# Performance work log

Hardware: AMD Instinct MI355X
Metric: run time of the kernel (lower is better)

The kernel has to match this reference:

```python
import jax, jax.numpy as jnp
import numpy as np

C = 64
EPS = 1e-5


def conv3x3(x, w, groups=1):
    # x: NCHW, w: OIHW, stride 1, padding 1, dilation 1 (matches the torch code)
    return jax.lax.conv_general_dilated(
        x, w, window_strides=(1, 1), padding=((1, 1), (1, 1)),
        dimension_numbers=('NCHW', 'OIHW', 'NCHW'), feature_group_count=groups)


def shared_conv(x, w_shared):
    # SharedConv: one (1,1,3,3) filter applied to every channel == depthwise conv
    # with the weight broadcast across channels (replaces the per-channel loop).
    w = jnp.broadcast_to(w_shared, (C, 1, 3, 3))
    return conv3x3(x, w, groups=C)


def sdc(x, w_sh, w_d, b_d):
    s = shared_conv(x, w_sh)
    d = conv3x3(s + x, w_d) + b_d[None, :, None, None]
    return d + x


def batch_norm(x, gamma, beta):
    # training-mode BatchNorm2d: batch statistics over (N, H, W), biased var
    mean = jnp.mean(x, axis=(0, 2, 3), keepdims=True)
    var = jnp.var(x, axis=(0, 2, 3), keepdims=True)
    xn = (x - mean) * jax.lax.rsqrt(var + EPS)
    return gamma[None, :, None, None] * xn + beta[None, :, None, None]


def setup_inputs() -> dict:
    key = jax.random.key(0)
    ks = jax.random.split(key, 7)
    fan_sh = 1 * 3 * 3
    fan_d = C * 3 * 3
    inp = {
        'x': jax.random.normal(ks[0], (4, C, 224, 224), dtype=jnp.float32),
        'w_sh1': jax.random.normal(ks[1], (1, 1, 3, 3), dtype=jnp.float32) / np.sqrt(fan_sh),
        'w_d1': jax.random.normal(ks[2], (C, C, 3, 3), dtype=jnp.float32) / np.sqrt(fan_d),
        'b_d1': jnp.zeros((C,), dtype=jnp.float32),
        'w_sh2': jax.random.normal(ks[3], (1, 1, 3, 3), dtype=jnp.float32) / np.sqrt(fan_sh),
        'w_d2': jax.random.normal(ks[4], (C, C, 3, 3), dtype=jnp.float32) / np.sqrt(fan_d),
        'b_d2': jnp.zeros((C,), dtype=jnp.float32),
        'gamma1': jnp.ones((C,), dtype=jnp.float32),
        'beta1': jnp.zeros((C,), dtype=jnp.float32),
        'gamma2': jnp.ones((C,), dtype=jnp.float32),
        'beta2': jnp.zeros((C,), dtype=jnp.float32),
    }
    return inp


def reference(x, w_sh1, w_d1, b_d1, w_sh2, w_d2, b_d2, gamma1, beta1, gamma2, beta2):
    o1 = sdc(x, w_sh1, w_d1, b_d1)
    o1 = jax.nn.relu(batch_norm(o1, gamma1, beta1))
    o2 = sdc(o1, w_sh2, w_d2, b_d2)
    o2 = jax.nn.relu(batch_norm(o2, gamma2, beta2))
    return o2 + x
```

## Files before the change

### kernel.cpp

```cpp
#include <hip/hip_runtime.h>

#define N_ 4
#define C_ 64
#define H_ 224
#define W_ 224
#define HW_ (H_ * W_)
#define CHW_ (C_ * HW_)
#define TOT_ (N_ * CHW_)

typedef __bf16 bf8 __attribute__((ext_vector_type(8)));
typedef float  f4v __attribute__((ext_vector_type(4)));
typedef unsigned short u16;

__device__ __forceinline__ float relu_(float v) { return fmaxf(v, 0.f); }
__device__ __forceinline__ u16 f2bf(float f) {
    unsigned u = __builtin_bit_cast(unsigned, f);
    return (u16)((u + 0x7FFFu + ((u >> 16) & 1u)) >> 16);
}
__device__ __forceinline__ float bf2f(u16 h) {
    unsigned u = ((unsigned)h) << 16;
    return __builtin_bit_cast(float, u);
}
__device__ __forceinline__ float bflo(unsigned u) {
    return __builtin_bit_cast(float, u << 16);
}
__device__ __forceinline__ float bfhi(unsigned u) {
    return __builtin_bit_cast(float, u & 0xFFFF0000u);
}

__global__ __launch_bounds__(256) void prep_w(
    const float* __restrict__ wd1, const float* __restrict__ wd2,
    u16* __restrict__ wpre)
{
    int i = blockIdx.x * 256 + threadIdx.x;
    if (i >= 73728) return;
    int sel = i >= 36864;
    int r   = i - sel * 36864;
    int tap = r >> 12;
    int r2  = r & 4095;
    int o   = r2 >> 6, k = r2 & 63;
    const float* ws = sel ? wd2 : wd1;
    wpre[i] = f2bf(ws[o * 576 + k * 9 + tap]);
}

__global__ __launch_bounds__(256) void tpass1(
    const float* __restrict__ x, const float* __restrict__ wsh,
    u16* __restrict__ th)
{
    __shared__ unsigned TL[32][36];

    float wk[9];
#pragma unroll
    for (int k = 0; k < 9; ++k) wk[k] = wsh[k];
    const float wc1 = wk[4] + 1.f;

    const int orig = blockIdx.x;
    const int swz  = (orig & 7) * 784 + (orig >> 3);
    const int n    = swz / 1568;
    const int rem  = swz - n * 1568;
    const int row  = rem / 7;
    const int strip = rem - row * 7;

    const int tid = threadIdx.x;
    const int qd = tid & 7;
    const int c2 = tid >> 3;
    const int w0 = strip * 32 + qd * 4;
    const bool ym = row > 0, yp = row < H_ - 1;
    const bool xm = w0 > 0, xp = w0 + 4 < W_;

    float tq[2][4];
#pragma unroll
    for (int s = 0; s < 2; ++s) {
        const int ch = c2 * 2 + s;
        const float* bp = x + (size_t)n * CHW_ + (size_t)ch * HW_ + row * W_ + w0;

        float m0[4] = {0,0,0,0}, m1[4], m2[4] = {0,0,0,0};
        float l0 = 0.f, r0 = 0.f, l1 = 0.f, r1 = 0.f, l2 = 0.f, r2 = 0.f;
        if (ym) {
            float4 v = *(const float4*)(bp - W_);
            m0[0] = v.x; m0[1] = v.y; m0[2] = v.z; m0[3] = v.w;
            if (xm) l0 = bp[-W_ - 1];
            if (xp) r0 = bp[-W_ + 4];
        }
        {
            float4 v = *(const float4*)bp;
            m1[0] = v.x; m1[1] = v.y; m1[2] = v.z; m1[3] = v.w;
            if (xm) l1 = bp[-1];
            if (xp) r1 = bp[4];
        }
        if (yp) {
            float4 v = *(const float4*)(bp + W_);
            m2[0] = v.x; m2[1] = v.y; m2[2] = v.z; m2[3] = v.w;
            if (xm) l2 = bp[W_ - 1];
            if (xp) r2 = bp[W_ + 4];
        }
#pragma unroll
        for (int j = 0; j < 4; ++j) {
            float a0 = (j == 0) ? l0 : m0[j - 1];
            float a2 = (j == 3) ? r0 : m0[j + 1];
            float b0 = (j == 0) ? l1 : m1[j - 1];
            float b2 = (j == 3) ? r1 : m1[j + 1];
            float c0 = (j == 0) ? l2 : m2[j - 1];
            float c2v = (j == 3) ? r2 : m2[j + 1];
            float t = wc1 * m1[j];
            t = fmaf(wk[0], a0,    t);
            t = fmaf(wk[1], m0[j], t);
            t = fmaf(wk[2], a2,    t);
            t = fmaf(wk[3], b0,    t);
            t = fmaf(wk[5], b2,    t);
            t = fmaf(wk[6], c0,    t);
            t = fmaf(wk[7], m2[j], t);
            t = fmaf(wk[8], c2v,   t);
            tq[s][j] = t;
        }
    }
#pragma unroll
    for (int j = 0; j < 4; ++j)
        TL[qd * 4 + j][c2] = (unsigned)f2bf(tq[0][j]) | ((unsigned)f2bf(tq[1][j]) << 16);
    __syncthreads();

    const int px = tid >> 3, s = tid & 7;
    uint4 v = *(const uint4*)&TL[px][s * 4];
    *(uint4*)(th + (size_t)(n * HW_ + row * W_ + strip * 32 + px) * 64 + s * 8) = v;
}

__global__ __launch_bounds__(256) void tpass2(
    const u16* __restrict__ inh, const float* __restrict__ wsh,
    const float* __restrict__ ss, u16* __restrict__ th)
{
    float wk[9];
#pragma unroll
    for (int k = 0; k < 9; ++k) wk[k] = wsh[k];
    const float wc1 = wk[4] + 1.f;

    const int f0 = blockIdx.x * 256 + threadIdx.x;
    const int s = f0 & 7;
    const int c0 = s * 8;
    float sc[8], sh[8];
#pragma unroll
    for (int j = 0; j < 8; ++j) { sc[j] = ss[c0 + j]; sh[j] = ss[64 + c0 + j]; }

    const int gsz = gridDim.x * 256;
    const int up = -64 * W_, dn = 64 * W_;

    for (int f = f0; f < TOT_ / 8; f += gsz) {
        const int pp = f >> 3;
        const int pix = pp % HW_;
        const int gh = pix / W_, gw = pix - gh * W_;
        const bool ym = gh > 0, yp = gh < H_ - 1, xm = gw > 0, xp = gw < W_ - 1;
        const u16* b = inh + (size_t)pp * 64 + c0;

        float t[8] = { 0.f, 0.f, 0.f, 0.f, 0.f, 0.f, 0.f, 0.f };
        auto acc8 = [&](int off, float wgt) {
            uint4 v = *(const uint4*)(b + off);
            unsigned wd_[4] = { v.x, v.y, v.z, v.w };
#pragma unroll
            for (int j = 0; j < 4; ++j) {
                float lo = bflo(wd_[j]), hi = bfhi(wd_[j]);
                t[2 * j]     = fmaf(wgt, relu_(fmaf(sc[2 * j], lo, sh[2 * j])), t[2 * j]);
                t[2 * j + 1] = fmaf(wgt, relu_(fmaf(sc[2 * j + 1], hi, sh[2 * j + 1])), t[2 * j + 1]);
            }
        };
        acc8(0, wc1);
        if (ym && xm) acc8(up - 64, wk[0]);
        if (ym)       acc8(up,      wk[1]);
        if (ym && xp) acc8(up + 64, wk[2]);
        if (xm)       acc8(-64,     wk[3]);
        if (xp)       acc8(64,      wk[5]);
        if (yp && xm) acc8(dn - 64, wk[6]);
        if (yp)       acc8(dn,      wk[7]);
        if (yp && xp) acc8(dn + 64, wk[8]);

        uint4 pk;
        pk.x = (unsigned)f2bf(t[0]) | ((unsigned)f2bf(t[1]) << 16);
        pk.y = (unsigned)f2bf(t[2]) | ((unsigned)f2bf(t[3]) << 16);
        pk.z = (unsigned)f2bf(t[4]) | ((unsigned)f2bf(t[5]) << 16);
        pk.w = (unsigned)f2bf(t[6]) | ((unsigned)f2bf(t[7]) << 16);
        *(uint4*)(th + (size_t)pp * 64 + c0) = pk;
    }
}

template<int LAYER>
__global__ __launch_bounds__(256, 3) void conv_mfma(
    const u16* __restrict__ th, const u16* __restrict__ wpre,
    const float* __restrict__ bd, const float* __restrict__ ss,
    const float* __restrict__ resx, const u16* __restrict__ reso,
    u16* __restrict__ dsth, float* __restrict__ dstf,
    float* __restrict__ raw)
{
    __shared__ __align__(16) char TlB[340 * 128];
    __shared__ float Sr[128];

    const int tid = threadIdx.x;
    const int n = blockIdx.z, h0 = blockIdx.y * 8, w0 = blockIdx.x * 32;
    const int lane = tid & 63, wg = tid >> 6;
    const int l15 = lane & 15, lg = lane >> 4;
    const int o = wg * 16 + l15;

    bf8 B[18];
#pragma unroll
    for (int tap = 0; tap < 9; ++tap)
#pragma unroll
        for (int cc = 0; cc < 2; ++cc)
            B[tap * 2 + cc] = *(const bf8*)(wpre + ((tap * 64 + o) * 64 + cc * 32 + lg * 8));

    for (int f = tid; f < 2720; f += 256) {
        int pix = f >> 3, s = f & 7;
        int hr = pix / 34, wc = pix - hr * 34;
        int gh = h0 - 1 + hr, gw = w0 - 1 + wc;
        float4 v = { 0.f, 0.f, 0.f, 0.f };
        if ((unsigned)gh < (unsigned)H_ && (unsigned)gw < (unsigned)W_)
            v = *(const float4*)(th + (size_t)(n * HW_ + gh * W_ + gw) * 64 + s * 8);
        *(float4*)(TlB + pix * 128 + ((s * 16) ^ ((pix & 7) << 4))) = v;
    }
    __syncthreads();

    f4v acc[16];
#pragma unroll
    for (int mf = 0; mf < 16; ++mf) acc[mf] = (f4v){0.f, 0.f, 0.f, 0.f};

#pragma unroll
    for (int mf = 0; mf < 16; ++mf) {
        const int h = mf >> 1, half = mf & 1;
#pragma unroll
        for (int tap = 0; tap < 9; ++tap) {
            const int dr = tap / 3, dc = tap - dr * 3;
            const int hp = (h + dr) * 34 + half * 16 + dc + l15;
#pragma unroll
            for (int cc = 0; cc < 2; ++cc) {
                const bf8 A = *(const bf8*)(TlB + hp * 128 +
                                            ((cc * 64 + lg * 16) ^ ((hp & 7) << 4)));
                acc[mf] = __builtin_amdgcn_mfma_f32_16x16x32_bf16(
                    A, B[tap * 2 + cc], acc[mf], 0, 0, 0);
            }
        }
    }

    const float bv = bd[o];
    float scO = 1.f, shO = 0.f;
    if (LAYER == 2) { scO = ss[o]; shO = ss[64 + o]; }
    float ps1 = 0.f, ps2 = 0.f;
#pragma unroll
    for (int mf = 0; mf < 16; ++mf) {
        const int h = h0 + (mf >> 1);
        const int w = w0 + (mf & 1) * 16 + lg * 4;
        const int ppix = n * HW_ + h * W_ + w;
        float vo[4];
        if (LAYER == 1) {
            const float4 rx = *(const float4*)(resx + (size_t)n * CHW_ + (size_t)o * HW_ + h * W_ + w);
            vo[0] = acc[mf][0] + bv + rx.x;
            vo[1] = acc[mf][1] + bv + rx.y;
            vo[2] = acc[mf][2] + bv + rx.z;
            vo[3] = acc[mf][3] + bv + rx.w;
#pragma unroll
            for (int r = 0; r < 4; ++r)
                dsth[(size_t)(ppix + r) * 64 + o] = f2bf(vo[r]);
        } else {
#pragma unroll
            for (int r = 0; r < 4; ++r) {
                float n1 = relu_(fmaf(scO, bf2f(reso[(size_t)(ppix + r) * 64 + o]), shO));
                vo[r] = acc[mf][r] + bv + n1;
            }
            float4 st = { vo[0], vo[1], vo[2], vo[3] };
            *(float4*)(dstf + (size_t)n * CHW_ + (size_t)o * HW_ + h * W_ + w) = st;
        }
        ps1 += (vo[0] + vo[1]) + (vo[2] + vo[3]);
        ps2 += fmaf(vo[0], vo[0], fmaf(vo[1], vo[1], fmaf(vo[2], vo[2], vo[3] * vo[3])));
    }
    ps1 += __shfl_xor(ps1, 16); ps1 += __shfl_xor(ps1, 32);
    ps2 += __shfl_xor(ps2, 16); ps2 += __shfl_xor(ps2, 32);
    if (lane < 16) { Sr[o] = ps1; Sr[64 + o] = ps2; }
    __syncthreads();
    if (tid < 128) atomicAdd(&raw[tid], Sr[tid]);
}

__global__ void stats_fin(const float* __restrict__ raw, const float* __restrict__ gamma,
                          const float* __restrict__ beta, float* __restrict__ ss)
{
    int c = threadIdx.x;
    if (c < 64) {
        const float cnt = (float)(N_ * HW_);
        float mean = raw[c] / cnt;
        float var  = raw[64 + c] / cnt - mean * mean;
        float inv  = rsqrtf(var + 1e-5f);
        float sc   = gamma[c] * inv;
        ss[c]      = sc;
        ss[64 + c] = fmaf(-sc, mean, beta[c]);
    }
}

__global__ __launch_bounds__(256) void final_k(
    float4* io, const float* __restrict__ ss, const float4* __restrict__ x)
{
    const int nq = TOT_ / 4;
    for (int i = blockIdx.x * 256 + threadIdx.x; i < nq; i += gridDim.x * 256) {
        int c = (i / (HW_ / 4)) & 63;
        float sc = ss[c], sh = ss[64 + c];
        float4 v = io[i], xx = x[i];
        float4 rr;
        rr.x = relu_(fmaf(sc, v.x, sh)) + xx.x;
        rr.y = relu_(fmaf(sc, v.y, sh)) + xx.y;
        rr.z = relu_(fmaf(sc, v.z, sh)) + xx.z;
        rr.w = relu_(fmaf(sc, v.w, sh)) + xx.w;
        io[i] = rr;
    }
}

extern "C" void kernel_launch(void* const* d_in, const int* in_sizes, int n_in,
                              void* d_out, int out_size, void* d_ws, size_t ws_size,
                              hipStream_t stream)
{
    const float* x    = (const float*)d_in[0];
    const float* wsh1 = (const float*)d_in[1];
    const float* wd1  = (const float*)d_in[2];
    const float* bd1  = (const float*)d_in[3];
    const float* wsh2 = (const float*)d_in[4];
    const float* wd2  = (const float*)d_in[5];
    const float* bd2  = (const float*)d_in[6];
    const float* g1   = (const float*)d_in[7];
    const float* be1  = (const float*)d_in[8];
    const float* g2   = (const float*)d_in[9];
    const float* be2  = (const float*)d_in[10];

    float* out = (float*)d_out;
    u16* Th   = (u16*)d_ws;
    u16* O1h  = Th + TOT_;
    u16* Wpre = O1h + TOT_;
    float* raw1 = (float*)(Wpre + 73728);
    float* raw2 = raw1 + 128;
    float* ss1  = raw2 + 128;
    float* ss2  = ss1 + 128;

    hipMemsetAsync(raw1, 0, 256 * sizeof(float), stream);
    prep_w<<<288, 256, 0, stream>>>(wd1, wd2, Wpre);

    const int t1grid = N_ * H_ * 7;
    dim3 cgrid(W_ / 32, H_ / 8, N_);

    tpass1<<<t1grid, 256, 0, stream>>>(x, wsh1, Th);
    conv_mfma<1><<<cgrid, 256, 0, stream>>>(Th, Wpre, bd1, nullptr, x, nullptr,
                                            O1h, nullptr, raw1);
    stats_fin<<<1, 64, 0, stream>>>(raw1, g1, be1, ss1);
    tpass2<<<2048, 256, 0, stream>>>(O1h, wsh2, ss1, Th);
    conv_mfma<2><<<cgrid, 256, 0, stream>>>(Th, Wpre + 36864, bd2, ss1, nullptr, O1h,
                                            nullptr, out, raw2);
    stats_fin<<<1, 64, 0, stream>>>(raw2, g2, be2, ss2);
    final_k<<<1024, 256, 0, stream>>>((float4*)out, ss2, (const float4*)x);
}
```

Baseline: 183.8 us.

## Store layer-1 intermediate in channel-planar bf16 and tile tpass2 like tpass1

The layer-1 conv epilogue now writes its bf16 output in NCHW order with one vectorized 4-pixel store, replacing scattered 2-byte stores to the pixel-major layout. The second layer's residual read is vectorized to match. tpass2 is rewritten to mirror tpass1: each block handles one row strip, does the normalized 3x3 shared conv per channel from planar data, and transposes through LDS to pixel-major output. It uses a swizzled block mapping. The aim is coalesced writes in the conv epilogue and fewer redundant neighbour loads in tpass2, at the cost of an LDS transpose and halo loads.

```diff
diff --git a/kernel.cpp b/kernel.cpp
--- a/kernel.cpp
+++ b/kernel.cpp
@@ -20,12 +20,6 @@
 __device__ __forceinline__ float bf2f(u16 h) {
     unsigned u = ((unsigned)h) << 16;
     return __builtin_bit_cast(float, u);
-}
-__device__ __forceinline__ float bflo(unsigned u) {
-    return __builtin_bit_cast(float, u << 16);
-}
-__device__ __forceinline__ float bfhi(unsigned u) {
-    return __builtin_bit_cast(float, u & 0xFFFF0000u);
 }
 
 __global__ __launch_bounds__(256) void prep_w(
@@ -125,59 +119,86 @@
 }
 
 __global__ __launch_bounds__(256) void tpass2(
-    const u16* __restrict__ inh, const float* __restrict__ wsh,
+    const u16* __restrict__ o1, const float* __restrict__ wsh,
     const float* __restrict__ ss, u16* __restrict__ th)
 {
+    __shared__ unsigned TL[32][36];
+
     float wk[9];
 #pragma unroll
     for (int k = 0; k < 9; ++k) wk[k] = wsh[k];
     const float wc1 = wk[4] + 1.f;
 
-    const int f0 = blockIdx.x * 256 + threadIdx.x;
-    const int s = f0 & 7;
-    const int c0 = s * 8;
-    float sc[8], sh[8];
-#pragma unroll
-    for (int j = 0; j < 8; ++j) { sc[j] = ss[c0 + j]; sh[j] = ss[64 + c0 + j]; }
-
-    const int gsz = gridDim.x * 256;
-    const int up = -64 * W_, dn = 64 * W_;
-
-    for (int f = f0; f < TOT_ / 8; f += gsz) {
-        const int pp = f >> 3;
-        const int pix = pp % HW_;
-        const int gh = pix / W_, gw = pix - gh * W_;
-        const bool ym = gh > 0, yp = gh < H_ - 1, xm = gw > 0, xp = gw < W_ - 1;
-        const u16* b = inh + (size_t)pp * 64 + c0;
-
-        float t[8] = { 0.f, 0.f, 0.f, 0.f, 0.f, 0.f, 0.f, 0.f };
-        auto acc8 = [&](int off, float wgt) {
-            uint4 v = *(const uint4*)(b + off);
-            unsigned wd_[4] = { v.x, v.y, v.z, v.w };
-#pragma unroll
-            for (int j = 0; j < 4; ++j) {
-                float lo = bflo(wd_[j]), hi = bfhi(wd_[j]);
-                t[2 * j]     = fmaf(wgt, relu_(fmaf(sc[2 * j], lo, sh[2 * j])), t[2 * j]);
-                t[2 * j + 1] = fmaf(wgt, relu_(fmaf(sc[2 * j + 1], hi, sh[2 * j + 1])), t[2 * j + 1]);
-            }
-        };
-        acc8(0, wc1);
-        if (ym && xm) acc8(up - 64, wk[0]);
-        if (ym)       acc8(up,      wk[1]);
-        if (ym && xp) acc8(up + 64, wk[2]);
-        if (xm)       acc8(-64,     wk[3]);
-        if (xp)       acc8(64,      wk[5]);
-        if (yp && xm) acc8(dn - 64, wk[6]);
-        if (yp)       acc8(dn,      wk[7]);
-        if (yp && xp) acc8(dn + 64, wk[8]);
-
-        uint4 pk;
-        pk.x = (unsigned)f2bf(t[0]) | ((unsigned)f2bf(t[1]) << 16);
-        pk.y = (unsigned)f2bf(t[2]) | ((unsigned)f2bf(t[3]) << 16);
-        pk.z = (unsigned)f2bf(t[4]) | ((unsigned)f2bf(t[5]) << 16);
-        pk.w = (unsigned)f2bf(t[6]) | ((unsigned)f2bf(t[7]) << 16);
-        *(uint4*)(th + (size_t)pp * 64 + c0) = pk;
-    }
+    const int orig = blockIdx.x;
+    const int swz  = (orig & 7) * 784 + (orig >> 3);
+    const int n    = swz / 1568;
+    const int rem  = swz - n * 1568;
+    const int row  = rem / 7;
+    const int strip = rem - row * 7;
+
+    const int tid = threadIdx.x;
+    const int qd = tid & 7;
+    const int c2 = tid >> 3;
+    const int w0 = strip * 32 + qd * 4;
+    const bool ym = row > 0, yp = row < H_ - 1;
+    const bool xm = w0 > 0, xp = w0 + 4 < W_;
+
+    float tq[2][4];
+#pragma unroll
+    for (int s = 0; s < 2; ++s) {
+        const int ch = c2 * 2 + s;
+        const float sc = ss[ch], sh = ss[64 + ch];
+        const u16* bp = o1 + (size_t)n * CHW_ + (size_t)ch * HW_ + row * W_ + w0;
+
+        float m0[4] = {0,0,0,0}, m1[4], m2[4] = {0,0,0,0};
+        float l0 = 0.f, r0 = 0.f, l1 = 0.f, r1 = 0.f, l2 = 0.f, r2 = 0.f;
+        auto nrm = [&](u16 u) { return relu_(fmaf(sc, bf2f(u), sh)); };
+        if (ym) {
+            ushort4 v = *(const ushort4*)(bp - W_);
+            m0[0] = nrm(v.x); m0[1] = nrm(v.y); m0[2] = nrm(v.z); m0[3] = nrm(v.w);
+            if (xm) l0 = nrm(bp[-W_ - 1]);
+            if (xp) r0 = nrm(bp[-W_ + 4]);
+        }
+        {
+            ushort4 v = *(const ushort4*)bp;
+            m1[0] = nrm(v.x); m1[1] = nrm(v.y); m1[2] = nrm(v.z); m1[3] = nrm(v.w);
+            if (xm) l1 = nrm(bp[-1]);
+            if (xp) r1 = nrm(bp[4]);
+        }
+        if (yp) {
+            ushort4 v = *(const ushort4*)(bp + W_);
+            m2[0] = nrm(v.x); m2[1] = nrm(v.y); m2[2] = nrm(v.z); m2[3] = nrm(v.w);
+            if (xm) l2 = nrm(bp[W_ - 1]);
+            if (xp) r2 = nrm(bp[W_ + 4]);
+        }
+#pragma unroll
+        for (int j = 0; j < 4; ++j) {
+            float a0 = (j == 0) ? l0 : m0[j - 1];
+            float a2 = (j == 3) ? r0 : m0[j + 1];
+            float b0 = (j == 0) ? l1 : m1[j - 1];
+            float b2 = (j == 3) ? r1 : m1[j + 1];
+            float c0 = (j == 0) ? l2 : m2[j - 1];
+            float c2v = (j == 3) ? r2 : m2[j + 1];
+            float t = wc1 * m1[j];
+            t = fmaf(wk[0], a0,    t);
+            t = fmaf(wk[1], m0[j], t);
+            t = fmaf(wk[2], a2,    t);
+            t = fmaf(wk[3], b0,    t);
+            t = fmaf(wk[5], b2,    t);
+            t = fmaf(wk[6], c0,    t);
+            t = fmaf(wk[7], m2[j], t);
+            t = fmaf(wk[8], c2v,   t);
+            tq[s][j] = t;
+        }
+    }
+#pragma unroll
+    for (int j = 0; j < 4; ++j)
+        TL[qd * 4 + j][c2] = (unsigned)f2bf(tq[0][j]) | ((unsigned)f2bf(tq[1][j]) << 16);
+    __syncthreads();
+
+    const int px = tid >> 3, s = tid & 7;
+    uint4 v = *(const uint4*)&TL[px][s * 4];
+    *(uint4*)(th + (size_t)(n * HW_ + row * W_ + strip * 32 + px) * 64 + s * 8) = v;
 }
 
 template<int LAYER>
@@ -244,25 +265,24 @@
     for (int mf = 0; mf < 16; ++mf) {
         const int h = h0 + (mf >> 1);
         const int w = w0 + (mf & 1) * 16 + lg * 4;
-        const int ppix = n * HW_ + h * W_ + w;
+        const size_t cidx = (size_t)n * CHW_ + (size_t)o * HW_ + h * W_ + w;
         float vo[4];
         if (LAYER == 1) {
-            const float4 rx = *(const float4*)(resx + (size_t)n * CHW_ + (size_t)o * HW_ + h * W_ + w);
+            const float4 rx = *(const float4*)(resx + cidx);
             vo[0] = acc[mf][0] + bv + rx.x;
             vo[1] = acc[mf][1] + bv + rx.y;
             vo[2] = acc[mf][2] + bv + rx.z;
             vo[3] = acc[mf][3] + bv + rx.w;
-#pragma unroll
-            for (int r = 0; r < 4; ++r)
-                dsth[(size_t)(ppix + r) * 64 + o] = f2bf(vo[r]);
+            ushort4 st = { f2bf(vo[0]), f2bf(vo[1]), f2bf(vo[2]), f2bf(vo[3]) };
+            *(ushort4*)(dsth + cidx) = st;
         } else {
-#pragma unroll
-            for (int r = 0; r < 4; ++r) {
-                float n1 = relu_(fmaf(scO, bf2f(reso[(size_t)(ppix + r) * 64 + o]), shO));
-                vo[r] = acc[mf][r] + bv + n1;
-            }
+            const ushort4 rv = *(const ushort4*)(reso + cidx);
+            vo[0] = acc[mf][0] + bv + relu_(fmaf(scO, bf2f(rv.x), shO));
+            vo[1] = acc[mf][1] + bv + relu_(fmaf(scO, bf2f(rv.y), shO));
+            vo[2] = acc[mf][2] + bv + relu_(fmaf(scO, bf2f(rv.z), shO));
+            vo[3] = acc[mf][3] + bv + relu_(fmaf(scO, bf2f(rv.w), shO));
             float4 st = { vo[0], vo[1], vo[2], vo[3] };
-            *(float4*)(dstf + (size_t)n * CHW_ + (size_t)o * HW_ + h * W_ + w) = st;
+            *(float4*)(dstf + cidx) = st;
         }
         ps1 += (vo[0] + vo[1]) + (vo[2] + vo[3]);
         ps2 += fmaf(vo[0], vo[0], fmaf(vo[1], vo[1], fmaf(vo[2], vo[2], vo[3] * vo[3])));
@@ -341,7 +361,7 @@
     conv_mfma<1><<<cgrid, 256, 0, stream>>>(Th, Wpre, bd1, nullptr, x, nullptr,
                                             O1h, nullptr, raw1);
     stats_fin<<<1, 64, 0, stream>>>(raw1, g1, be1, ss1);
-    tpass2<<<2048, 256, 0, stream>>>(O1h, wsh2, ss1, Th);
+    tpass2<<<t1grid, 256, 0, stream>>>(O1h, wsh2, ss1, Th);
     conv_mfma<2><<<cgrid, 256, 0, stream>>>(Th, Wpre + 36864, bd2, ss1, nullptr, O1h,
                                             nullptr, out, raw2);
     stats_fin<<<1, 64, 0, stream>>>(raw2, g2, be2, ss2);
```

After: 222.5 us. 21.1% more time.

## Fold BN finalize into consumers, halve conv tile, stream weights per tap

Applied to the files above, without the earlier changes.

Removes the two stats_fin launches by recomputing the BatchNorm scale/shift in shared memory inside tpass2, conv_mfma<2> and final_k. The MFMA conv tile shrinks from 8 to 4 rows, which cuts LDS and accumulator registers. The 18 preloaded weight fragments are replaced by a per-tap double-buffered global load with the tap loop kept rolled, and launch bounds are raised to 4 blocks per CU to get more occupancy. The cost is more halo reloads per output, redundant stats math in every block, and weight loads now inside the main loop.

```diff
diff --git a/kernel.cpp b/kernel.cpp
--- a/kernel.cpp
+++ b/kernel.cpp
@@ -126,19 +126,33 @@
 
 __global__ __launch_bounds__(256) void tpass2(
     const u16* __restrict__ inh, const float* __restrict__ wsh,
-    const float* __restrict__ ss, u16* __restrict__ th)
-{
+    const float* __restrict__ raw, const float* __restrict__ gamma,
+    const float* __restrict__ beta, u16* __restrict__ th)
+{
+    __shared__ float SS[128];
+    const int tid = threadIdx.x;
+    if (tid < 64) {
+        const float cnt = (float)(N_ * HW_);
+        float mean = raw[tid] / cnt;
+        float var  = raw[64 + tid] / cnt - mean * mean;
+        float inv  = rsqrtf(var + 1e-5f);
+        float scv  = gamma[tid] * inv;
+        SS[tid]      = scv;
+        SS[64 + tid] = fmaf(-scv, mean, beta[tid]);
+    }
+    __syncthreads();
+
     float wk[9];
 #pragma unroll
     for (int k = 0; k < 9; ++k) wk[k] = wsh[k];
     const float wc1 = wk[4] + 1.f;
 
-    const int f0 = blockIdx.x * 256 + threadIdx.x;
+    const int f0 = blockIdx.x * 256 + tid;
     const int s = f0 & 7;
     const int c0 = s * 8;
     float sc[8], sh[8];
 #pragma unroll
-    for (int j = 0; j < 8; ++j) { sc[j] = ss[c0 + j]; sh[j] = ss[64 + c0 + j]; }
+    for (int j = 0; j < 8; ++j) { sc[j] = SS[c0 + j]; sh[j] = SS[64 + c0 + j]; }
 
     const int gsz = gridDim.x * 256;
     const int up = -64 * W_, dn = 64 * W_;
@@ -181,30 +195,36 @@
 }
 
 template<int LAYER>
-__global__ __launch_bounds__(256, 3) void conv_mfma(
+__global__ __launch_bounds__(256, 4) void conv_mfma(
     const u16* __restrict__ th, const u16* __restrict__ wpre,
-    const float* __restrict__ bd, const float* __restrict__ ss,
+    const float* __restrict__ bd,
+    const float* __restrict__ rawin, const float* __restrict__ gamma,
+    const float* __restrict__ beta,
     const float* __restrict__ resx, const u16* __restrict__ reso,
     u16* __restrict__ dsth, float* __restrict__ dstf,
     float* __restrict__ raw)
 {
-    __shared__ __align__(16) char TlB[340 * 128];
+    __shared__ __align__(16) char TlB[204 * 128];
     __shared__ float Sr[128];
+    __shared__ float SS[128];
 
     const int tid = threadIdx.x;
-    const int n = blockIdx.z, h0 = blockIdx.y * 8, w0 = blockIdx.x * 32;
+    const int n = blockIdx.z, h0 = blockIdx.y * 4, w0 = blockIdx.x * 32;
     const int lane = tid & 63, wg = tid >> 6;
     const int l15 = lane & 15, lg = lane >> 4;
     const int o = wg * 16 + l15;
 
-    bf8 B[18];
-#pragma unroll
-    for (int tap = 0; tap < 9; ++tap)
-#pragma unroll
-        for (int cc = 0; cc < 2; ++cc)
-            B[tap * 2 + cc] = *(const bf8*)(wpre + ((tap * 64 + o) * 64 + cc * 32 + lg * 8));
-
-    for (int f = tid; f < 2720; f += 256) {
+    if (LAYER == 2 && tid < 64) {
+        const float cnt = (float)(N_ * HW_);
+        float mean = rawin[tid] / cnt;
+        float var  = rawin[64 + tid] / cnt - mean * mean;
+        float inv  = rsqrtf(var + 1e-5f);
+        float scv  = gamma[tid] * inv;
+        SS[tid]      = scv;
+        SS[64 + tid] = fmaf(-scv, mean, beta[tid]);
+    }
+
+    for (int f = tid; f < 1632; f += 256) {
         int pix = f >> 3, s = f & 7;
         int hr = pix / 34, wc = pix - hr * 34;
         int gh = h0 - 1 + hr, gw = w0 - 1 + wc;
@@ -215,39 +235,47 @@
     }
     __syncthreads();
 
-    f4v acc[16];
-#pragma unroll
-    for (int mf = 0; mf < 16; ++mf) acc[mf] = (f4v){0.f, 0.f, 0.f, 0.f};
-
-#pragma unroll
-    for (int mf = 0; mf < 16; ++mf) {
-        const int h = mf >> 1, half = mf & 1;
-#pragma unroll
-        for (int tap = 0; tap < 9; ++tap) {
-            const int dr = tap / 3, dc = tap - dr * 3;
-            const int hp = (h + dr) * 34 + half * 16 + dc + l15;
-#pragma unroll
-            for (int cc = 0; cc < 2; ++cc) {
-                const bf8 A = *(const bf8*)(TlB + hp * 128 +
-                                            ((cc * 64 + lg * 16) ^ ((hp & 7) << 4)));
-                acc[mf] = __builtin_amdgcn_mfma_f32_16x16x32_bf16(
-                    A, B[tap * 2 + cc], acc[mf], 0, 0, 0);
-            }
-        }
+    f4v acc[8];
+#pragma unroll
+    for (int mf = 0; mf < 8; ++mf) acc[mf] = (f4v){0.f, 0.f, 0.f, 0.f};
+
+    const u16* wb = wpre + o * 64 + lg * 8;
+    bf8 B0 = *(const bf8*)(wb);
+    bf8 B1 = *(const bf8*)(wb + 32);
+#pragma unroll 1
+    for (int tap = 0; tap < 9; ++tap) {
+        bf8 nB0, nB1;
+        if (tap < 8) {
+            nB0 = *(const bf8*)(wb + (tap + 1) * 4096);
+            nB1 = *(const bf8*)(wb + (tap + 1) * 4096 + 32);
+        }
+        const int dr = tap / 3, dc = tap - dr * 3;
+#pragma unroll
+        for (int mf = 0; mf < 8; ++mf) {
+            const int hp = ((mf >> 1) + dr) * 34 + (mf & 1) * 16 + dc + l15;
+            const bf8 A0 = *(const bf8*)(TlB + hp * 128 +
+                                         ((lg * 16) ^ ((hp & 7) << 4)));
+            acc[mf] = __builtin_amdgcn_mfma_f32_16x16x32_bf16(A0, B0, acc[mf], 0, 0, 0);
+            const bf8 A1 = *(const bf8*)(TlB + hp * 128 +
+                                         ((64 + lg * 16) ^ ((hp & 7) << 4)));
+            acc[mf] = __builtin_amdgcn_mfma_f32_16x16x32_bf16(A1, B1, acc[mf], 0, 0, 0);
+        }
+        B0 = nB0; B1 = nB1;
     }
 
     const float bv = bd[o];
     float scO = 1.f, shO = 0.f;
-    if (LAYER == 2) { scO = ss[o]; shO = ss[64 + o]; }
+    if (LAYER == 2) { scO = SS[o]; shO = SS[64 + o]; }
     float ps1 = 0.f, ps2 = 0.f;
 #pragma unroll
-    for (int mf = 0; mf < 16; ++mf) {
+    for (int mf = 0; mf < 8; ++mf) {
         const int h = h0 + (mf >> 1);
         const int w = w0 + (mf & 1) * 16 + lg * 4;
         const int ppix = n * HW_ + h * W_ + w;
+        const size_t cidx = (size_t)n * CHW_ + (size_t)o * HW_ + h * W_ + w;
         float vo[4];
         if (LAYER == 1) {
-            const float4 rx = *(const float4*)(resx + (size_t)n * CHW_ + (size_t)o * HW_ + h * W_ + w);
+            const float4 rx = *(const float4*)(resx + cidx);
             vo[0] = acc[mf][0] + bv + rx.x;
             vo[1] = acc[mf][1] + bv + rx.y;
             vo[2] = acc[mf][2] + bv + rx.z;
@@ -262,7 +290,7 @@
                 vo[r] = acc[mf][r] + bv + n1;
             }
             float4 st = { vo[0], vo[1], vo[2], vo[3] };
-            *(float4*)(dstf + (size_t)n * CHW_ + (size_t)o * HW_ + h * W_ + w) = st;
+            *(float4*)(dstf + cidx) = st;
         }
         ps1 += (vo[0] + vo[1]) + (vo[2] + vo[3]);
         ps2 += fmaf(vo[0], vo[0], fmaf(vo[1], vo[1], fmaf(vo[2], vo[2], vo[3] * vo[3])));
@@ -274,28 +302,27 @@
     if (tid < 128) atomicAdd(&raw[tid], Sr[tid]);
 }
 
-__global__ void stats_fin(const float* __restrict__ raw, const float* __restrict__ gamma,
-                          const float* __restrict__ beta, float* __restrict__ ss)
-{
-    int c = threadIdx.x;
-    if (c < 64) {
+__global__ __launch_bounds__(256) void final_k(
+    float4* io, const float* __restrict__ raw, const float* __restrict__ gamma,
+    const float* __restrict__ beta, const float4* __restrict__ x)
+{
+    __shared__ float SS[128];
+    if (threadIdx.x < 64) {
+        const int c = threadIdx.x;
         const float cnt = (float)(N_ * HW_);
         float mean = raw[c] / cnt;
         float var  = raw[64 + c] / cnt - mean * mean;
         float inv  = rsqrtf(var + 1e-5f);
-        float sc   = gamma[c] * inv;
-        ss[c]      = sc;
-        ss[64 + c] = fmaf(-sc, mean, beta[c]);
-    }
-}
-
-__global__ __launch_bounds__(256) void final_k(
-    float4* io, const float* __restrict__ ss, const float4* __restrict__ x)
-{
+        float scv  = gamma[c] * inv;
+        SS[c]      = scv;
+        SS[64 + c] = fmaf(-scv, mean, beta[c]);
+    }
+    __syncthreads();
+
     const int nq = TOT_ / 4;
     for (int i = blockIdx.x * 256 + threadIdx.x; i < nq; i += gridDim.x * 256) {
         int c = (i / (HW_ / 4)) & 63;
-        float sc = ss[c], sh = ss[64 + c];
+        float sc = SS[c], sh = SS[64 + c];
         float4 v = io[i], xx = x[i];
         float4 rr;
         rr.x = relu_(fmaf(sc, v.x, sh)) + xx.x;
@@ -328,22 +355,20 @@
     u16* Wpre = O1h + TOT_;
     float* raw1 = (float*)(Wpre + 73728);
     float* raw2 = raw1 + 128;
-    float* ss1  = raw2 + 128;
-    float* ss2  = ss1 + 128;
 
     hipMemsetAsync(raw1, 0, 256 * sizeof(float), stream);
     prep_w<<<288, 256, 0, stream>>>(wd1, wd2, Wpre);
 
     const int t1grid = N_ * H_ * 7;
-    dim3 cgrid(W_ / 32, H_ / 8, N_);
+    dim3 cgrid(W_ / 32, H_ / 4, N_);
 
     tpass1<<<t1grid, 256, 0, stream>>>(x, wsh1, Th);
-    conv_mfma<1><<<cgrid, 256, 0, stream>>>(Th, Wpre, bd1, nullptr, x, nullptr,
-                                            O1h, nullptr, raw1);
-    stats_fin<<<1, 64, 0, stream>>>(raw1, g1, be1, ss1);
-    tpass2<<<2048, 256, 0, stream>>>(O1h, wsh2, ss1, Th);
-    conv_mfma<2><<<cgrid, 256, 0, stream>>>(Th, Wpre + 36864, bd2, ss1, nullptr, O1h,
-                                            nullptr, out, raw2);
-    stats_fin<<<1, 64, 0, stream>>>(raw2, g2, be2, ss2);
-    final_k<<<1024, 256, 0, stream>>>((float4*)out, ss2, (const float4*)x);
-}
+    conv_mfma<1><<<cgrid, 256, 0, stream>>>(Th, Wpre, bd1,
+                                            nullptr, nullptr, nullptr,
+                                            x, nullptr, O1h, nullptr, raw1);
+    tpass2<<<2048, 256, 0, stream>>>(O1h, wsh2, raw1, g1, be1, Th);
+    conv_mfma<2><<<cgrid, 256, 0, stream>>>(Th, Wpre + 36864, bd2,
+                                            raw1, g1, be1,
+                                            nullptr, O1h, nullptr, out, raw2);
+    final_k<<<2048, 256, 0, stream>>>((float4*)out, raw2, g2, be2, (const float4*)x);
+}
```

New measurement: 205.1 us. 11.6% more time.
